# Optimization experiments

Hardware: AMD Instinct MI355X
Metric: run time of the kernel (lower is better)

## Reference

```python
import jax, jax.numpy as jnp
import numpy as np
import math

N, I, C, T, V, M = 256, 2, 6, 300, 25, 2
D = 256
IN_DIM = I * C * T * V * M  # 180000


def _const_mats():
    a = math.radians(30.0)
    ca, sa = math.cos(a), math.sin(a)
    R_x = np.array([[1, 0, 0], [0, ca, sa], [0, -sa, ca]], np.float32).T
    R_y = np.array([[ca, 0, -sa], [0, 1, 0], [sa, 0, ca]], np.float32).T
    R_z = np.array([[ca, sa, 0], [-sa, ca, 0], [0, 0, 1]], np.float32).T
    R_rotate = R_x @ R_y @ R_z
    R_scale = np.diag([2.0, 2.0, 2.0]).astype(np.float32)
    R_shear = np.ones((3, 3), np.float32)  # sh_next=1 -> all ones (transpose is identity op)
    return R_rotate, R_shear, R_scale


def _param_mats():
    rotate_w = np.zeros((3, 3), np.float32)
    rotate_w[0, 0] = 1.0
    rotate_w[1, 1] = rotate_w[1, 2] = rotate_w[2, 1] = rotate_w[2, 2] = 0.7
    shear_w = np.full((3, 3), 0.8, np.float32)
    np.fill_diagonal(shear_w, 1.0)
    scale_w = np.diag([0.6, 0.6, 0.6]).astype(np.float32)
    return rotate_w, shear_w, scale_w


def setup_inputs() -> dict:
    key = jax.random.key(0)
    k1, k2 = jax.random.split(key)
    R_rotate, R_shear, R_scale = _const_mats()
    rotate_w, shear_w, scale_w = _param_mats()
    x = jax.random.normal(k1, (N, I, C, T, V, M), jnp.float32)
    W = jax.random.normal(k2, (IN_DIM, D), jnp.float32) * (1.0 / math.sqrt(IN_DIM))
    b = jnp.zeros((D,), jnp.float32)
    return {
        "x": x,
        "rotate_weight": jnp.asarray(rotate_w),
        "shear_weight": jnp.asarray(shear_w),
        "scale_weight": jnp.asarray(scale_w),
        "W_backbone": W,
        "b_backbone": b,
        "R_rotate": jnp.asarray(R_rotate),
        "R_shear": jnp.asarray(R_shear),
        "R_scale": jnp.asarray(R_scale),
    }


def _loss_fn(q, z, n):
    q = q / jnp.linalg.norm(q, axis=-1, keepdims=True)
    z = z / jnp.linalg.norm(z, axis=-1, keepdims=True)
    sim = q @ z.T                       # [N, N]
    diag = jnp.diagonal(sim)            # (q*z).sum(-1)
    offdiag_sum = sim.sum(axis=-1) - diag
    return diag - offdiag_sum / (n - 1)


def reference(x, rotate_weight, shear_weight, scale_weight, W_backbone, b_backbone,
              R_rotate, R_shear, R_scale):
    n, i, c, t, v, m = x.shape
    # per-pass effective 3x3 matrices (elementwise gated constants)
    Rr = R_rotate * rotate_weight
    Rs = R_shear * shear_weight
    Rc = R_scale * scale_weight
    Rtot = Rr @ Rs @ Rc  # sequential passes compose: y @ Rr @ Rs @ Rc
    # split C=6 into two xyz chunks, rotate coord axis (vectorized over N,I,chunk,T,V,M)
    xr = x.reshape(n, i, 2, 3, t, v, m)
    x_aug = jnp.einsum("nhctvm,cd->nhdtvm", xr.reshape(n * i, 2 * 0 + 2, 3, t, v, m)[0:0] if False else xr.reshape(n, i * 2, 3, t, v, m), Rtot)
    x_aug = x_aug.reshape(n, i, c, t, v, m)
    # torch x1 = x aliases: x2 == x1 == augmented tensor -> both branches identical
    feats = x_aug.reshape(n, -1)
    z = feats @ W_backbone + b_backbone  # backbone; projector(num_layers=0) is identity
    out = z                              # out1 == out2 == z
    q = z                                # predictor is identity
    z_d = jax.lax.stop_gradient(z)
    loss = _loss_fn(q, z_d, n) + _loss_fn(q, z_d, n)
    return (loss.mean(), out, out)
```

## Files before the change

### kernel.cpp

```cpp
#include <hip/hip_runtime.h>

typedef __attribute__((ext_vector_type(4))) short bf16x4;
typedef __attribute__((ext_vector_type(8))) short bf16x8;
typedef __attribute__((ext_vector_type(16))) float f32x16;
typedef __attribute__((ext_vector_type(2))) float f32x2;
typedef __attribute__((ext_vector_type(4))) unsigned int u32x4;

__device__ __forceinline__ unsigned short f2bf(float f) {
    unsigned int u = __builtin_bit_cast(unsigned int, f);
    u += 0x7fffu + ((u >> 16) & 1u);
    return (unsigned short)(u >> 16);
}

#define PA 196

__global__ __launch_bounds__(512, 2) void gemm_kernel(
    const float* __restrict__ x,
    const float* __restrict__ rw, const float* __restrict__ sw, const float* __restrict__ cw,
    const float* __restrict__ W,
    const float* __restrict__ Rr, const float* __restrict__ Rs, const float* __restrict__ Rc,
    float* __restrict__ P)
{
    __shared__ unsigned short lds_a[256 * PA];
    __shared__ unsigned int   lds_b[2][16 * 256];

    const int tid = threadIdx.x;
    const int blk = blockIdx.x;
    const int p0 = blk * 60;

    float Ar[9], Br[9], Cr[9], T1[9], RT[9];
    #pragma unroll
    for (int e = 0; e < 9; ++e) {
        Ar[e] = Rr[e] * rw[e];
        Br[e] = Rs[e] * sw[e];
        Cr[e] = Rc[e] * cw[e];
    }
    #pragma unroll
    for (int r = 0; r < 3; ++r)
        #pragma unroll
        for (int c = 0; c < 3; ++c)
            T1[r*3+c] = Ar[r*3+0]*Br[0*3+c] + Ar[r*3+1]*Br[1*3+c] + Ar[r*3+2]*Br[2*3+c];
    #pragma unroll
    for (int r = 0; r < 3; ++r)
        #pragma unroll
        for (int c = 0; c < 3; ++c)
            RT[r*3+c] = T1[r*3+0]*Cr[0*3+c] + T1[r*3+1]*Cr[1*3+c] + T1[r*3+2]*Cr[2*3+c];

    if (tid < 256) {
        bf16x4 zz = (bf16x4)0;
        #pragma unroll
        for (int c3 = 0; c3 < 3; ++c3)
            *((bf16x4*)&lds_a[tid*PA + c3*64 + 60]) = zz;
    }

    const int w  = tid >> 6, l = tid & 63;
    const int lm = l & 31,  lh = l >> 5;
    const int m0 = (w >> 1) * 64;
    const int d0 = (w & 1) * 128;

    f32x16 acc[2][4];
    #pragma unroll
    for (int fm = 0; fm < 2; ++fm)
        #pragma unroll
        for (int fd = 0; fd < 4; ++fd)
            acc[fm][fd] = (f32x16)0.0f;

    for (int s = 0; s < 4; ++s) {
        const int i = s >> 1, chunk = s & 1;
        const long kbase = (long)i * 90000 + (long)chunk * 45000 + p0;
        const float* xs = x + kbase;

        f32x2 L0[4], L1[4];
        int bd[4], bvk2[4];
        #pragma unroll
        for (int jj = 0; jj < 4; ++jj) {
            int item = jj*512 + tid;
            int vk2l = item >> 7, dp = item & 127;
            int vk = vk2l*2;
            int c3 = vk >> 6, pl = vk & 63;
            bd[jj] = dp*2; bvk2[jj] = vk2l;
            L0[jj] = (f32x2){0.f,0.f}; L1[jj] = (f32x2){0.f,0.f};
            if (pl < 60) {
                const float* wr = W + (kbase + (long)c3*15000 + pl)*256 + dp*2;
                L0[jj] = *(const f32x2*)wr;
                L1[jj] = *(const f32x2*)(wr + 256);
            }
        }

        #pragma unroll 6
        for (int j = 0; j < 30; ++j) {
            int q = j*512 + tid;
            int n = (int)(((unsigned)q * 34953u) >> 21);
            int pl = q - n*60;
            const float* px = xs + (long)n*180000 + pl;
            float x0 = px[0], x1 = px[15000], x2 = px[30000];
            float f0 = x0*RT[0] + x1*RT[3] + x2*RT[6];
            float f1 = x0*RT[1] + x1*RT[4] + x2*RT[7];
            float f2 = x0*RT[2] + x1*RT[5] + x2*RT[8];
            int a = n*PA + pl;
            lds_a[a      ] = f2bf(f0);
            lds_a[a +  64] = f2bf(f1);
            lds_a[a + 128] = f2bf(f2);
        }

        #pragma unroll
        for (int jj = 0; jj < 4; ++jj) {
            unsigned int lo = (unsigned int)f2bf(L0[jj].x) | ((unsigned int)f2bf(L1[jj].x) << 16);
            unsigned int hi = (unsigned int)f2bf(L0[jj].y) | ((unsigned int)f2bf(L1[jj].y) << 16);
            unsigned int* pb = &lds_b[0][bvk2[jj]*256 + bd[jj]];
            pb[0] = lo; pb[1] = hi;
        }
        __syncthreads();

        for (int t = 0; t < 6; ++t) {
            f32x2 M0[4], M1[4];
            int cd[4], cvk2[4];
            const bool have = (t < 5);
            if (have) {
                #pragma unroll
                for (int jj = 0; jj < 4; ++jj) {
                    int item = jj*512 + tid;
                    int vk2l = item >> 7, dp = item & 127;
                    int vk = (t+1)*32 + vk2l*2;
                    int c3 = vk >> 6, pl = vk & 63;
                    cd[jj] = dp*2; cvk2[jj] = vk2l;
                    M0[jj] = (f32x2){0.f,0.f}; M1[jj] = (f32x2){0.f,0.f};
                    if (pl < 60) {
                        const float* wr = W + (kbase + (long)c3*15000 + pl)*256 + dp*2;
                        M0[jj] = *(const f32x2*)wr;
                        M1[jj] = *(const f32x2*)(wr + 256);
                    }
                }
            }

            const unsigned int* bbuf = lds_b[t & 1];
            #pragma unroll
            for (int kk = 0; kk < 2; ++kk) {
                int vk0 = t*32 + kk*16;
                int kb = vk0 + lh*8;
                bf16x8 af[2];
                #pragma unroll
                for (int fm = 0; fm < 2; ++fm) {
                    const unsigned short* pa = &lds_a[(m0 + fm*32 + lm)*PA + kb];
                    bf16x4 alo = *(const bf16x4*)pa;
                    bf16x4 ahi = *(const bf16x4*)(pa + 4);
                    af[fm] = __builtin_shufflevector(alo, ahi, 0,1,2,3,4,5,6,7);
                }
                #pragma unroll
                for (int fd = 0; fd < 4; ++fd) {
                    int db = d0 + fd*32 + lm;
                    int v2 = kk*8 + lh*4;
                    u32x4 bw = { bbuf[(v2+0)*256 + db], bbuf[(v2+1)*256 + db],
                                 bbuf[(v2+2)*256 + db], bbuf[(v2+3)*256 + db] };
                    bf16x8 bfv = __builtin_bit_cast(bf16x8, bw);
                    #pragma unroll
                    for (int fm = 0; fm < 2; ++fm)
                        acc[fm][fd] = __builtin_amdgcn_mfma_f32_32x32x16_bf16(af[fm], bfv, acc[fm][fd], 0, 0, 0);
                }
            }

            if (have) {
                unsigned int* nb = &lds_b[(t+1) & 1][0];
                #pragma unroll
                for (int jj = 0; jj < 4; ++jj) {
                    unsigned int lo = (unsigned int)f2bf(M0[jj].x) | ((unsigned int)f2bf(M1[jj].x) << 16);
                    unsigned int hi = (unsigned int)f2bf(M0[jj].y) | ((unsigned int)f2bf(M1[jj].y) << 16);
                    unsigned int* pb = &nb[cvk2[jj]*256 + cd[jj]];
                    pb[0] = lo; pb[1] = hi;
                }
            }
            __syncthreads();
        }
    }

    float* Pb = P + (size_t)blk * 65536;
    #pragma unroll
    for (int fm = 0; fm < 2; ++fm)
        #pragma unroll
        for (int fd = 0; fd < 4; ++fd)
            #pragma unroll
            for (int r = 0; r < 16; ++r) {
                int row = m0 + fm*32 + (r & 3) + 8*(r >> 2) + 4*lh;
                int col = d0 + fd*32 + lm;
                Pb[row*256 + col] = acc[fm][fd][r];
            }
}

__global__ __launch_bounds__(1024) void reduce_kernel(
    const float* __restrict__ P, const float* __restrict__ bias,
    float* __restrict__ out, float* __restrict__ Z)
{
    __shared__ float sred[4][256];
    __shared__ float wsum[16];
    const int n = blockIdx.x;
    const int tid = threadIdx.x;
    const int sg = tid >> 8, d = tid & 255;

    const float* p = P + (size_t)n*256 + d;
    float z = 0.f;
    #pragma unroll 8
    for (int s = sg; s < 250; s += 4) z += p[(size_t)s * 65536];
    sred[sg][d] = z;
    __syncthreads();

    float zf = 0.f;
    if (sg == 0) zf = sred[0][d] + sred[1][d] + sred[2][d] + sred[3][d] + bias[d];
    float sq = zf * zf;
    #pragma unroll
    for (int off = 32; off > 0; off >>= 1) sq += __shfl_down(sq, off, 64);
    if ((tid & 63) == 0) wsum[tid >> 6] = sq;
    __syncthreads();
    if (sg == 0) {
        float tot = wsum[0] + wsum[1] + wsum[2] + wsum[3];
        float inv = rsqrtf(tot);
        out[1 + n*256 + d]         = zf;
        out[1 + 65536 + n*256 + d] = zf;
        Z[n*256 + d] = zf * inv;
    }
}

__global__ __launch_bounds__(1024) void loss_kernel(const float* __restrict__ Z, float* __restrict__ out)
{
    __shared__ float sp[4][256];
    __shared__ float w4[16];
    const int tid = threadIdx.x;
    const int g = tid >> 8, d = tid & 255;
    float S = 0.f;
    #pragma unroll 8
    for (int n = g*64; n < g*64 + 64; ++n) S += Z[n*256 + d];
    sp[g][d] = S;
    __syncthreads();
    float v = 0.f;
    if (g == 0) {
        S = sp[0][d] + sp[1][d] + sp[2][d] + sp[3][d];
        v = S * S;
    }
    #pragma unroll
    for (int off = 32; off > 0; off >>= 1) v += __shfl_down(v, off, 64);
    if ((tid & 63) == 0) w4[tid >> 6] = v;
    __syncthreads();
    if (tid == 0) {
        float tot = w4[0] + w4[1] + w4[2] + w4[3];
        out[0] = 2.0f - (2.0f / 255.0f) * (tot * (1.0f / 256.0f) - 1.0f);
    }
}

extern "C" void kernel_launch(void* const* d_in, const int* in_sizes, int n_in,
                              void* d_out, int out_size, void* d_ws, size_t ws_size,
                              hipStream_t stream)
{
    (void)in_sizes; (void)n_in; (void)out_size; (void)ws_size;
    const float* x  = (const float*)d_in[0];
    const float* rw = (const float*)d_in[1];
    const float* sw = (const float*)d_in[2];
    const float* cw = (const float*)d_in[3];
    const float* W  = (const float*)d_in[4];
    const float* bb = (const float*)d_in[5];
    const float* Rr = (const float*)d_in[6];
    const float* Rs = (const float*)d_in[7];
    const float* Rc = (const float*)d_in[8];
    float* out = (float*)d_out;
    float* P = (float*)d_ws;
    float* Z = P + (size_t)250 * 65536;

    gemm_kernel<<<250, 512, 0, stream>>>(x, rw, sw, cw, W, Rr, Rs, Rc, P);
    reduce_kernel<<<256, 1024, 0, stream>>>(P, bb, out, Z);
    loss_kernel<<<1, 1024, 0, stream>>>(Z, out);
}
```

Baseline: 407.6 us.

## Double GEMM block to 1024 threads with 128-bit loads and vectorized reductions

The GEMM block grows from 512 to 1024 threads, so 16 waves each own a 64x64 output tile instead of 8 waves owning 64x128. The x and W staging now uses float4 global loads and 128-bit LDS stores in place of scalar or float2 accesses. The reduce and loss kernels switch to float4 accumulation with xor shuffles. The aim is more latency hiding and fewer memory instructions, at the cost of only one block per CU, since LDS use is about 130KB, and each wave now reads A fragments for half as many MFMAs.

```diff
diff --git a/kernel.cpp b/kernel.cpp
--- a/kernel.cpp
+++ b/kernel.cpp
@@ -3,7 +3,7 @@
 typedef __attribute__((ext_vector_type(4))) short bf16x4;
 typedef __attribute__((ext_vector_type(8))) short bf16x8;
 typedef __attribute__((ext_vector_type(16))) float f32x16;
-typedef __attribute__((ext_vector_type(2))) float f32x2;
+typedef __attribute__((ext_vector_type(4))) float f32x4;
 typedef __attribute__((ext_vector_type(4))) unsigned int u32x4;
 
 __device__ __forceinline__ unsigned short f2bf(float f) {
@@ -14,7 +14,7 @@
 
 #define PA 196
 
-__global__ __launch_bounds__(512, 2) void gemm_kernel(
+__global__ __launch_bounds__(1024) void gemm_kernel(
     const float* __restrict__ x,
     const float* __restrict__ rw, const float* __restrict__ sw, const float* __restrict__ cw,
     const float* __restrict__ W,
@@ -26,15 +26,11 @@
 
     const int tid = threadIdx.x;
     const int blk = blockIdx.x;
-    const int p0 = blk * 60;
+    const int p0  = blk * 60;
 
     float Ar[9], Br[9], Cr[9], T1[9], RT[9];
     #pragma unroll
-    for (int e = 0; e < 9; ++e) {
-        Ar[e] = Rr[e] * rw[e];
-        Br[e] = Rs[e] * sw[e];
-        Cr[e] = Rc[e] * cw[e];
-    }
+    for (int e = 0; e < 9; ++e) { Ar[e] = Rr[e]*rw[e]; Br[e] = Rs[e]*sw[e]; Cr[e] = Rc[e]*cw[e]; }
     #pragma unroll
     for (int r = 0; r < 3; ++r)
         #pragma unroll
@@ -55,89 +51,94 @@
 
     const int w  = tid >> 6, l = tid & 63;
     const int lm = l & 31,  lh = l >> 5;
-    const int m0 = (w >> 1) * 64;
-    const int d0 = (w & 1) * 128;
-
-    f32x16 acc[2][4];
+    const int m0 = (w >> 2) * 64;
+    const int d0 = (w & 3) * 64;
+    const int kp = tid >> 6;
+    const int d4 = tid & 63;
+
+    f32x16 acc[2][2];
     #pragma unroll
     for (int fm = 0; fm < 2; ++fm)
         #pragma unroll
-        for (int fd = 0; fd < 4; ++fd)
+        for (int fd = 0; fd < 2; ++fd)
             acc[fm][fd] = (f32x16)0.0f;
 
     for (int s = 0; s < 4; ++s) {
-        const int i = s >> 1, chunk = s & 1;
-        const long kbase = (long)i * 90000 + (long)chunk * 45000 + p0;
+        const long kbase = (long)(s >> 1) * 90000 + (long)(s & 1) * 45000 + p0;
         const float* xs = x + kbase;
 
-        f32x2 L0[4], L1[4];
-        int bd[4], bvk2[4];
-        #pragma unroll
-        for (int jj = 0; jj < 4; ++jj) {
-            int item = jj*512 + tid;
-            int vk2l = item >> 7, dp = item & 127;
-            int vk = vk2l*2;
+        f32x4 L0 = (f32x4)0.f, L1 = (f32x4)0.f;
+        {
+            int vk = kp * 2;
             int c3 = vk >> 6, pl = vk & 63;
-            bd[jj] = dp*2; bvk2[jj] = vk2l;
-            L0[jj] = (f32x2){0.f,0.f}; L1[jj] = (f32x2){0.f,0.f};
             if (pl < 60) {
-                const float* wr = W + (kbase + (long)c3*15000 + pl)*256 + dp*2;
-                L0[jj] = *(const f32x2*)wr;
-                L1[jj] = *(const f32x2*)(wr + 256);
-            }
-        }
-
-        #pragma unroll 6
-        for (int j = 0; j < 30; ++j) {
-            int q = j*512 + tid;
-            int n = (int)(((unsigned)q * 34953u) >> 21);
-            int pl = q - n*60;
-            const float* px = xs + (long)n*180000 + pl;
-            float x0 = px[0], x1 = px[15000], x2 = px[30000];
-            float f0 = x0*RT[0] + x1*RT[3] + x2*RT[6];
-            float f1 = x0*RT[1] + x1*RT[4] + x2*RT[7];
-            float f2 = x0*RT[2] + x1*RT[5] + x2*RT[8];
-            int a = n*PA + pl;
-            lds_a[a      ] = f2bf(f0);
-            lds_a[a +  64] = f2bf(f1);
-            lds_a[a + 128] = f2bf(f2);
-        }
-
-        #pragma unroll
-        for (int jj = 0; jj < 4; ++jj) {
-            unsigned int lo = (unsigned int)f2bf(L0[jj].x) | ((unsigned int)f2bf(L1[jj].x) << 16);
-            unsigned int hi = (unsigned int)f2bf(L0[jj].y) | ((unsigned int)f2bf(L1[jj].y) << 16);
-            unsigned int* pb = &lds_b[0][bvk2[jj]*256 + bd[jj]];
-            pb[0] = lo; pb[1] = hi;
+                const float* wr = W + (kbase + (long)c3*15000 + pl)*256 + d4*4;
+                L0 = *(const f32x4*)wr;
+                L1 = *(const f32x4*)(wr + 256);
+            }
+        }
+
+        #pragma unroll
+        for (int h = 0; h < 2; ++h) {
+            f32x4 X[2][3];
+            int nn[2], pp[2]; bool act[2];
+            #pragma unroll
+            for (int u = 0; u < 2; ++u) {
+                int idx = (h*2 + u)*1024 + tid;
+                act[u] = idx < 3840;
+                int n = (int)(((unsigned)idx * 34953u) >> 19);
+                int p4 = idx - n*15;
+                nn[u] = n; pp[u] = p4;
+                if (act[u]) {
+                    const float* px = xs + (long)n*180000 + p4*4;
+                    X[u][0] = *(const f32x4*)px;
+                    X[u][1] = *(const f32x4*)(px + 15000);
+                    X[u][2] = *(const f32x4*)(px + 30000);
+                }
+            }
+            #pragma unroll
+            for (int u = 0; u < 2; ++u) {
+                if (!act[u]) continue;
+                bf16x4 o0, o1, o2;
+                #pragma unroll
+                for (int e = 0; e < 4; ++e) {
+                    float x0 = X[u][0][e], x1 = X[u][1][e], x2 = X[u][2][e];
+                    o0[e] = (short)f2bf(x0*RT[0] + x1*RT[3] + x2*RT[6]);
+                    o1[e] = (short)f2bf(x0*RT[1] + x1*RT[4] + x2*RT[7]);
+                    o2[e] = (short)f2bf(x0*RT[2] + x1*RT[5] + x2*RT[8]);
+                }
+                int a = nn[u]*PA + pp[u]*4;
+                *((bf16x4*)&lds_a[a      ]) = o0;
+                *((bf16x4*)&lds_a[a +  64]) = o1;
+                *((bf16x4*)&lds_a[a + 128]) = o2;
+            }
+        }
+
+        {
+            u32x4 bw;
+            #pragma unroll
+            for (int e = 0; e < 4; ++e)
+                bw[e] = (unsigned int)f2bf(L0[e]) | ((unsigned int)f2bf(L1[e]) << 16);
+            *((u32x4*)&lds_b[0][kp*256 + d4*4]) = bw;
         }
         __syncthreads();
 
         for (int t = 0; t < 6; ++t) {
-            f32x2 M0[4], M1[4];
-            int cd[4], cvk2[4];
-            const bool have = (t < 5);
-            if (have) {
-                #pragma unroll
-                for (int jj = 0; jj < 4; ++jj) {
-                    int item = jj*512 + tid;
-                    int vk2l = item >> 7, dp = item & 127;
-                    int vk = (t+1)*32 + vk2l*2;
-                    int c3 = vk >> 6, pl = vk & 63;
-                    cd[jj] = dp*2; cvk2[jj] = vk2l;
-                    M0[jj] = (f32x2){0.f,0.f}; M1[jj] = (f32x2){0.f,0.f};
-                    if (pl < 60) {
-                        const float* wr = W + (kbase + (long)c3*15000 + pl)*256 + dp*2;
-                        M0[jj] = *(const f32x2*)wr;
-                        M1[jj] = *(const f32x2*)(wr + 256);
-                    }
+            f32x4 M0 = (f32x4)0.f, M1 = (f32x4)0.f;
+            if (t < 5) {
+                int vk = (t+1)*32 + kp*2;
+                int c3 = vk >> 6, pl = vk & 63;
+                if (pl < 60) {
+                    const float* wr = W + (kbase + (long)c3*15000 + pl)*256 + d4*4;
+                    M0 = *(const f32x4*)wr;
+                    M1 = *(const f32x4*)(wr + 256);
                 }
             }
 
             const unsigned int* bbuf = lds_b[t & 1];
             #pragma unroll
             for (int kk = 0; kk < 2; ++kk) {
-                int vk0 = t*32 + kk*16;
-                int kb = vk0 + lh*8;
+                int kb = t*32 + kk*16 + lh*8;
                 bf16x8 af[2];
                 #pragma unroll
                 for (int fm = 0; fm < 2; ++fm) {
@@ -147,27 +148,24 @@
                     af[fm] = __builtin_shufflevector(alo, ahi, 0,1,2,3,4,5,6,7);
                 }
                 #pragma unroll
-                for (int fd = 0; fd < 4; ++fd) {
+                for (int fd = 0; fd < 2; ++fd) {
                     int db = d0 + fd*32 + lm;
                     int v2 = kk*8 + lh*4;
-                    u32x4 bw = { bbuf[(v2+0)*256 + db], bbuf[(v2+1)*256 + db],
-                                 bbuf[(v2+2)*256 + db], bbuf[(v2+3)*256 + db] };
-                    bf16x8 bfv = __builtin_bit_cast(bf16x8, bw);
+                    u32x4 bwv = { bbuf[(v2+0)*256 + db], bbuf[(v2+1)*256 + db],
+                                  bbuf[(v2+2)*256 + db], bbuf[(v2+3)*256 + db] };
+                    bf16x8 bfv = __builtin_bit_cast(bf16x8, bwv);
                     #pragma unroll
                     for (int fm = 0; fm < 2; ++fm)
                         acc[fm][fd] = __builtin_amdgcn_mfma_f32_32x32x16_bf16(af[fm], bfv, acc[fm][fd], 0, 0, 0);
                 }
             }
 
-            if (have) {
-                unsigned int* nb = &lds_b[(t+1) & 1][0];
-                #pragma unroll
-                for (int jj = 0; jj < 4; ++jj) {
-                    unsigned int lo = (unsigned int)f2bf(M0[jj].x) | ((unsigned int)f2bf(M1[jj].x) << 16);
-                    unsigned int hi = (unsigned int)f2bf(M0[jj].y) | ((unsigned int)f2bf(M1[jj].y) << 16);
-                    unsigned int* pb = &nb[cvk2[jj]*256 + cd[jj]];
-                    pb[0] = lo; pb[1] = hi;
-                }
+            if (t < 5) {
+                u32x4 bw;
+                #pragma unroll
+                for (int e = 0; e < 4; ++e)
+                    bw[e] = (unsigned int)f2bf(M0[e]) | ((unsigned int)f2bf(M1[e]) << 16);
+                *((u32x4*)&lds_b[(t+1) & 1][kp*256 + d4*4]) = bw;
             }
             __syncthreads();
         }
@@ -177,7 +175,7 @@
     #pragma unroll
     for (int fm = 0; fm < 2; ++fm)
         #pragma unroll
-        for (int fd = 0; fd < 4; ++fd)
+        for (int fd = 0; fd < 2; ++fd)
             #pragma unroll
             for (int r = 0; r < 16; ++r) {
                 int row = m0 + fm*32 + (r & 3) + 8*(r >> 2) + 4*lh;
@@ -186,62 +184,58 @@
             }
 }
 
-__global__ __launch_bounds__(1024) void reduce_kernel(
+__global__ __launch_bounds__(512) void reduce_kernel(
     const float* __restrict__ P, const float* __restrict__ bias,
     float* __restrict__ out, float* __restrict__ Z)
 {
-    __shared__ float sred[4][256];
-    __shared__ float wsum[16];
+    __shared__ f32x4 sred[8][64];
     const int n = blockIdx.x;
     const int tid = threadIdx.x;
-    const int sg = tid >> 8, d = tid & 255;
-
-    const float* p = P + (size_t)n*256 + d;
-    float z = 0.f;
+    const int d4 = tid & 63, sg = tid >> 6;
+
+    const f32x4* p = (const f32x4*)(P + (size_t)n * 256) + d4;
+    f32x4 z = (f32x4)0.f;
     #pragma unroll 8
-    for (int s = sg; s < 250; s += 4) z += p[(size_t)s * 65536];
-    sred[sg][d] = z;
+    for (int s = sg; s < 250; s += 8) z += p[(size_t)s * 16384];
+    sred[sg][d4] = z;
     __syncthreads();
 
-    float zf = 0.f;
-    if (sg == 0) zf = sred[0][d] + sred[1][d] + sred[2][d] + sred[3][d] + bias[d];
-    float sq = zf * zf;
-    #pragma unroll
-    for (int off = 32; off > 0; off >>= 1) sq += __shfl_down(sq, off, 64);
-    if ((tid & 63) == 0) wsum[tid >> 6] = sq;
+    if (tid < 64) {
+        f32x4 zf = sred[0][tid];
+        #pragma unroll
+        for (int g = 1; g < 8; ++g) zf += sred[g][tid];
+        zf += ((const f32x4*)bias)[tid];
+        float* o1 = out + 1 + n*256 + tid*4;
+        float* o2 = o1 + 65536;
+        #pragma unroll
+        for (int e = 0; e < 4; ++e) { o1[e] = zf[e]; o2[e] = zf[e]; }
+        float sq = zf[0]*zf[0] + zf[1]*zf[1] + zf[2]*zf[2] + zf[3]*zf[3];
+        #pragma unroll
+        for (int off = 32; off > 0; off >>= 1) sq += __shfl_xor(sq, off, 64);
+        float inv = rsqrtf(sq);
+        ((f32x4*)Z)[n*64 + tid] = zf * inv;
+    }
+}
+
+__global__ __launch_bounds__(1024) void loss_kernel(const float* __restrict__ Z, float* __restrict__ out)
+{
+    __shared__ f32x4 sp[16][64];
+    const int tid = threadIdx.x;
+    const int c4 = tid & 63, g = tid >> 6;
+    f32x4 S = (f32x4)0.f;
+    #pragma unroll 4
+    for (int n = g; n < 256; n += 16) S += ((const f32x4*)Z)[n*64 + c4];
+    sp[g][c4] = S;
     __syncthreads();
-    if (sg == 0) {
-        float tot = wsum[0] + wsum[1] + wsum[2] + wsum[3];
-        float inv = rsqrtf(tot);
-        out[1 + n*256 + d]         = zf;
-        out[1 + 65536 + n*256 + d] = zf;
-        Z[n*256 + d] = zf * inv;
-    }
-}
-
-__global__ __launch_bounds__(1024) void loss_kernel(const float* __restrict__ Z, float* __restrict__ out)
-{
-    __shared__ float sp[4][256];
-    __shared__ float w4[16];
-    const int tid = threadIdx.x;
-    const int g = tid >> 8, d = tid & 255;
-    float S = 0.f;
-    #pragma unroll 8
-    for (int n = g*64; n < g*64 + 64; ++n) S += Z[n*256 + d];
-    sp[g][d] = S;
-    __syncthreads();
-    float v = 0.f;
-    if (g == 0) {
-        S = sp[0][d] + sp[1][d] + sp[2][d] + sp[3][d];
-        v = S * S;
-    }
-    #pragma unroll
-    for (int off = 32; off > 0; off >>= 1) v += __shfl_down(v, off, 64);
-    if ((tid & 63) == 0) w4[tid >> 6] = v;
-    __syncthreads();
-    if (tid == 0) {
-        float tot = w4[0] + w4[1] + w4[2] + w4[3];
-        out[0] = 2.0f - (2.0f / 255.0f) * (tot * (1.0f / 256.0f) - 1.0f);
+    if (tid < 64) {
+        f32x4 T = sp[0][tid];
+        #pragma unroll
+        for (int gg = 1; gg < 16; ++gg) T += sp[gg][tid];
+        float v = T[0]*T[0] + T[1]*T[1] + T[2]*T[2] + T[3]*T[3];
+        #pragma unroll
+        for (int off = 32; off > 0; off >>= 1) v += __shfl_xor(v, off, 64);
+        if (tid == 0)
+            out[0] = 2.0f - (2.0f / 255.0f) * (v * (1.0f / 256.0f) - 1.0f);
     }
 }
 
@@ -263,7 +257,7 @@
     float* P = (float*)d_ws;
     float* Z = P + (size_t)250 * 65536;
 
-    gemm_kernel<<<250, 512, 0, stream>>>(x, rw, sw, cw, W, Rr, Rs, Rc, P);
-    reduce_kernel<<<256, 1024, 0, stream>>>(P, bb, out, Z);
+    gemm_kernel<<<250, 1024, 0, stream>>>(x, rw, sw, cw, W, Rr, Rs, Rc, P);
+    reduce_kernel<<<256, 512, 0, stream>>>(P, bb, out, Z);
     loss_kernel<<<1, 1024, 0, stream>>>(Z, out);
 }
```

Result: slower. 423.3 us (+3.8%).
